# Optimization experiments

Hardware: AMD Instinct MI355X
Metric: run time of the kernel (lower is better)

The kernel has to match this reference:

```python
import jax, jax.numpy as jnp
import numpy as np

E, D, H, K = 8, 768, 3072, 2   # num_experts, embed_size, expert_size, top-k
TAU = 1.0
BN, PN = 32, 196

def l2norm(v):
    # F.normalize(p=2, dim=-1), eps=1e-12
    return v / jnp.maximum(jnp.linalg.norm(v, axis=-1, keepdims=True), 1e-12)

def setup_inputs() -> dict:
    key = jax.random.key(0)
    ks = jax.random.split(key, 8)
    s = 0.02  # weight init scale for stability
    return {
        "x": jax.random.normal(ks[0], (BN, PN, D), dtype=jnp.float32),
        "Wlinear": jax.random.normal(ks[1], (D, D), dtype=jnp.float32) * s,
        "learnedE": jax.random.normal(ks[2], (E, D), dtype=jnp.float32),
        "bias": jnp.zeros((BN * PN, E), dtype=jnp.float32),
        "W1": jax.random.normal(ks[3], (E, D, H), dtype=jnp.float32) * s,
        "b1": jnp.zeros((E, H), dtype=jnp.float32),
        "W2": jax.random.normal(ks[4], (E, H, D), dtype=jnp.float32) * s,
        "b2": jnp.zeros((E, D), dtype=jnp.float32),
        "sW1": jax.random.normal(ks[5], (D, H), dtype=jnp.float32) * s,
        "sb1": jnp.zeros((H,), dtype=jnp.float32),
        "sW2": jax.random.normal(ks[6], (H, D), dtype=jnp.float32) * s,
        "sb2": jnp.zeros((D,), dtype=jnp.float32),
    }

def reference(x, Wlinear, learnedE, bias, W1, b1, W2, b2, sW1, sb1, sW2, sb2):
    bn, pn, d = x.shape
    patches = x.reshape(bn * pn, d)                      # [T, D]
    proj = l2norm(patches @ Wlinear.T)                   # router projection
    routed = proj @ l2norm(learnedE).T                   # [T, E] cosine scores
    probs = jax.nn.softmax((routed + bias) / TAU, axis=1)  # eval path (no noise)
    k_probs, k_idx = jax.lax.top_k(probs, K)             # [T, K]
    # combine weights: scatter top-k probs into dense [T, E] gate matrix
    T = probs.shape[0]
    gates = jnp.zeros_like(probs).at[jnp.arange(T)[:, None], k_idx].add(k_probs)
    # expert MLPs computed densely for all experts, masked by gates
    h = jax.nn.gelu(jnp.einsum('td,edh->teh', patches, W1) + b1[None], approximate=False)
    eo = jnp.einsum('teh,ehd->ted', h, W2) + b2[None]    # [T, E, D]
    moe = jnp.einsum('ted,te->td', eo, gates)            # weighted combine
    # shared expert (expert_list[-1]) applied to every token; dropout is identity in eval
    shared = jax.nn.gelu(patches @ sW1 + sb1, approximate=False) @ sW2 + sb2
    return (moe + shared).reshape(bn, pn, d)
```

## Files before the change

kernel.cpp:

```cpp
#include <hip/hip_runtime.h>
#include <hip/hip_bf16.h>

typedef __hip_bfloat16 bf16;
typedef __attribute__((ext_vector_type(8))) short short8;
typedef __attribute__((ext_vector_type(4))) float f32x4;

#define T_TOK 6272
#define D_DIM 768
#define H_DIM 3072
#define NEXP 8
#define MAXTILES 160

__device__ __forceinline__ void async16(void* lds, const void* g) {
  __builtin_amdgcn_global_load_lds(
      (const __attribute__((address_space(1))) void*)g,
      (__attribute__((address_space(3))) void*)lds, 16, 0, 0);
}

__device__ __forceinline__ float gelu_f(float x) {
  float z = x * 0.70710678118654752f;
  float az = fabsf(z);
  float t = 1.f / (1.f + 0.3275911f * az);
  float poly = ((((1.061405429f * t - 1.453152027f) * t + 1.421413741f) * t -
                 0.284496736f) * t + 0.254829592f) * t;
  float e = __expf(-az * az);
  float er = 1.f - poly * e;
  er = copysignf(er, z);
  return 0.5f * x * (1.f + er);
}


__global__ void cast_hilo(const float* __restrict__ in, bf16* __restrict__ hi,
                          bf16* __restrict__ lo, int n) {
  int i = blockIdx.x * blockDim.x + threadIdx.x;
  int stride = gridDim.x * blockDim.x;
  for (; i < n; i += stride) {
    float x = in[i];
    bf16 h = __float2bfloat16(x);
    hi[i] = h;
    lo[i] = __float2bfloat16(x - __bfloat162float(h));
  }
}

__global__ void transpose_cast(const float* __restrict__ in, bf16* __restrict__ out,
                               int R, int C) {
  __shared__ float tile[32][33];
  int b = blockIdx.z;
  const float* ib = in + (size_t)b * R * C;
  bf16* ob = out + (size_t)b * R * C;
  int r0 = blockIdx.x * 32, c0 = blockIdx.y * 32;
  int tx = threadIdx.x & 31, ty = threadIdx.x >> 5;
  for (int i = 0; i < 32; i += 8)
    tile[ty + i][tx] = ib[(size_t)(r0 + ty + i) * C + c0 + tx];
  __syncthreads();
  for (int i = 0; i < 32; i += 8)
    ob[(size_t)(c0 + ty + i) * R + r0 + tx] = __float2bfloat16(tile[tx][ty + i]);
}

__global__ void norm_learnedE(const float* __restrict__ lE, float* __restrict__ eHat) {
  int wave = threadIdx.x >> 6, lane = threadIdx.x & 63;
  for (int e = wave; e < NEXP; e += 4) {
    float v[12];
    float ss = 0.f;
    for (int j = 0; j < 12; j++) {
      v[j] = lE[e * D_DIM + lane + 64 * j];
      ss += v[j] * v[j];
    }
    for (int o = 32; o; o >>= 1) ss += __shfl_xor(ss, o);
    float rn = 1.f / fmaxf(sqrtf(ss), 1e-12f);
    for (int j = 0; j < 12; j++) eHat[e * D_DIM + lane + 64 * j] = v[j] * rn;
  }
}


__global__ __launch_bounds__(256) void gemm_router(
    const bf16* __restrict__ pHi, const bf16* __restrict__ pLo,
    const bf16* __restrict__ wHi, const bf16* __restrict__ wLo,
    float* __restrict__ y) {
  __shared__ __align__(16) bf16 As[2][128 * 32];
  __shared__ __align__(16) bf16 Bs[2][128 * 32];
  int tid = threadIdx.x, wave = tid >> 6, lane = tid & 63;
  int wr = wave >> 1, wc = wave & 1;
  int rowbase = blockIdx.x * 128, colbase = blockIdx.y * 128;
  int sc8 = (lane & 3) * 8;

  size_t aoff[2], boff[2];
  for (int p = 0; p < 2; p++) {
    int r = wave * 32 + p * 16 + (lane >> 2);
    aoff[p] = (size_t)(rowbase + r) * D_DIM + sc8;
    boff[p] = (size_t)(colbase + r) * D_DIM + sc8;
  }

  auto stage = [&](int buf, int ks) {
    int term = ks / 24;
    const bf16* A = (term == 1) ? pLo : pHi;
    const bf16* B = (term == 2) ? wLo : wHi;
    int kk = (ks - term * 24) * 32;
#pragma unroll
    for (int p = 0; p < 2; p++) {
      async16(&As[buf][(wave * 32 + p * 16) * 32], A + aoff[p] + kk);
      async16(&Bs[buf][(wave * 32 + p * 16) * 32], B + boff[p] + kk);
    }
  };

  f32x4 acc[4][4];
#pragma unroll
  for (int m = 0; m < 4; m++)
#pragma unroll
    for (int n = 0; n < 4; n++) acc[m][n] = 0.f;

  stage(0, 0);
  __syncthreads();
  int cur = 0;
  for (int ks = 0; ks < 72; ks++) {
    if (ks < 71) stage(cur ^ 1, ks + 1);
    int koff = (lane >> 4) * 8;
    const bf16* Ac = As[cur];
    const bf16* Bc = Bs[cur];
    short8 af[4], bfr[4];
#pragma unroll
    for (int m = 0; m < 4; m++)
      af[m] = *(const short8*)&Ac[(wr * 64 + m * 16 + (lane & 15)) * 32 + koff];
#pragma unroll
    for (int n = 0; n < 4; n++)
      bfr[n] = *(const short8*)&Bc[(wc * 64 + n * 16 + (lane & 15)) * 32 + koff];
#pragma unroll
    for (int m = 0; m < 4; m++)
#pragma unroll
      for (int n = 0; n < 4; n++)
        acc[m][n] = __builtin_amdgcn_mfma_f32_16x16x32_bf16(af[m], bfr[n], acc[m][n], 0, 0, 0);
    __syncthreads();
    cur ^= 1;
  }
  for (int m = 0; m < 4; m++)
    for (int n = 0; n < 4; n++)
      for (int j = 0; j < 4; j++) {
        int r = rowbase + wr * 64 + m * 16 + (lane >> 4) * 4 + j;
        int c = colbase + wc * 64 + n * 16 + (lane & 15);
        y[(size_t)r * D_DIM + c] = acc[m][n][j];
      }
}


__global__ void router_epi(const float* __restrict__ y, const float* __restrict__ eHat,
                           const float* __restrict__ bias, int* __restrict__ gidx,
                           float* __restrict__ gval, int* __restrict__ counts) {
  int wave = threadIdx.x >> 6, lane = threadIdx.x & 63;
  int t = blockIdx.x * 4 + wave;
  float v[12];
  float ss = 0.f;
  for (int j = 0; j < 12; j++) {
    v[j] = y[(size_t)t * D_DIM + lane + 64 * j];
    ss += v[j] * v[j];
  }
  for (int o = 32; o; o >>= 1) ss += __shfl_xor(ss, o);
  float d[NEXP];
  for (int e = 0; e < NEXP; e++) {
    float s = 0.f;
    for (int j = 0; j < 12; j++) s += v[j] * eHat[e * D_DIM + lane + 64 * j];
    for (int o = 32; o; o >>= 1) s += __shfl_xor(s, o);
    d[e] = s;
  }
  if (lane == 0) {
    float rn = 1.f / fmaxf(sqrtf(ss), 1e-12f);
    float sc[NEXP], mx = -1e30f;
    for (int e = 0; e < NEXP; e++) {
      sc[e] = d[e] * rn + bias[t * NEXP + e];
      mx = fmaxf(mx, sc[e]);
    }
    float p[NEXP], sum = 0.f;
    for (int e = 0; e < NEXP; e++) {
      p[e] = expf(sc[e] - mx);
      sum += p[e];
    }
    float inv = 1.f / sum;
    int i1 = 0;
    for (int e = 1; e < NEXP; e++)
      if (sc[e] > sc[i1]) i1 = e;
    int i2 = -1;
    for (int e = 0; e < NEXP; e++) {
      if (e == i1) continue;
      if (i2 < 0 || sc[e] > sc[i2]) i2 = e;
    }
    gidx[t * 2] = i1;
    gidx[t * 2 + 1] = i2;
    gval[t * 2] = p[i1] * inv;
    gval[t * 2 + 1] = p[i2] * inv;
    atomicAdd(&counts[i1], 1);
    atomicAdd(&counts[i2], 1);
  }
}


__global__ void scan_build(const int* __restrict__ counts, int* __restrict__ segstart,
                           int* __restrict__ cursors, int* __restrict__ tiles,
                           int* __restrict__ numtiles) {
  if (threadIdx.x == 0) {
    int off = 0;
    for (int e = 0; e < NEXP; e++) {
      segstart[e] = off;
      cursors[e] = off;
      off += counts[e];
    }
    segstart[NEXP] = off;
    segstart[NEXP + 1] = off + T_TOK;
    int nt = 0;
    for (int e = 0; e < NEXP + 1; e++) {
      int cnt = (e < NEXP) ? counts[e] : T_TOK;
      int ntl = (cnt + 127) >> 7;
      for (int l = 0; l < ntl; l++) {
        tiles[nt * 2] = e;
        tiles[nt * 2 + 1] = l;
        nt++;
      }
    }
    *numtiles = nt;
  }
}

__global__ void fill_assign(const int* __restrict__ gidx, int* __restrict__ cursors,
                            int* __restrict__ rowtok, int* __restrict__ slot_of) {
  int t = blockIdx.x * 256 + threadIdx.x;
  if (t >= T_TOK) return;
  for (int k = 0; k < 2; k++) {
    int e = gidx[t * 2 + k];
    int pos = atomicAdd(&cursors[e], 1);
    rowtok[pos] = t;
    slot_of[t * 2 + k] = pos;
  }
  rowtok[2 * T_TOK + t] = t;
}


__global__ __launch_bounds__(256) void gemm_ffn1(
    const bf16* __restrict__ pHi, const bf16* __restrict__ W1T,
    const bf16* __restrict__ sW1T, const float* __restrict__ b1,
    const float* __restrict__ sb1, const int* __restrict__ segstart,
    const int* __restrict__ tiles, const int* __restrict__ numtiles,
    const int* __restrict__ rowtok, bf16* __restrict__ hbuf) {
  int gx = blockIdx.x;
  if (gx >= *numtiles) return;
  int seg = tiles[gx * 2], lt = tiles[gx * 2 + 1];
  int s0 = segstart[seg] + lt * 128;
  int send = segstart[seg + 1];
  const bf16* Bw = (seg < NEXP) ? W1T + (size_t)seg * H_DIM * D_DIM : sW1T;
  const float* bb = (seg < NEXP) ? b1 + seg * H_DIM : sb1;

  __shared__ __align__(16) bf16 As[2][128 * 32];
  __shared__ __align__(16) bf16 Bs[2][128 * 32];
  int tid = threadIdx.x, wave = tid >> 6, lane = tid & 63;
  int wr = wave >> 1, wc = wave & 1;
  int colbase = blockIdx.y * 128;
  int sc8 = (lane & 3) * 8;

  const bf16* arow[2];
  const bf16* brow[2];
  for (int p = 0; p < 2; p++) {
    int r = wave * 32 + p * 16 + (lane >> 2);
    int s = s0 + r;
    if (s > send - 1) s = send - 1;
    arow[p] = pHi + (size_t)rowtok[s] * D_DIM + sc8;
    brow[p] = Bw + (size_t)(colbase + r) * D_DIM + sc8;
  }

  auto stage = [&](int buf, int ks) {
    int kk = ks * 32;
#pragma unroll
    for (int p = 0; p < 2; p++) {
      async16(&As[buf][(wave * 32 + p * 16) * 32], arow[p] + kk);
      async16(&Bs[buf][(wave * 32 + p * 16) * 32], brow[p] + kk);
    }
  };

  f32x4 acc[4][4];
#pragma unroll
  for (int m = 0; m < 4; m++)
#pragma unroll
    for (int n = 0; n < 4; n++) acc[m][n] = 0.f;

  stage(0, 0);
  __syncthreads();
  int cur = 0;
  for (int ks = 0; ks < 24; ks++) {
    if (ks < 23) stage(cur ^ 1, ks + 1);
    int koff = (lane >> 4) * 8;
    const bf16* Ac = As[cur];
    const bf16* Bc = Bs[cur];
    short8 af[4], bfr[4];
#pragma unroll
    for (int m = 0; m < 4; m++)
      af[m] = *(const short8*)&Ac[(wr * 64 + m * 16 + (lane & 15)) * 32 + koff];
#pragma unroll
    for (int n = 0; n < 4; n++)
      bfr[n] = *(const short8*)&Bc[(wc * 64 + n * 16 + (lane & 15)) * 32 + koff];
#pragma unroll
    for (int m = 0; m < 4; m++)
#pragma unroll
      for (int n = 0; n < 4; n++)
        acc[m][n] = __builtin_amdgcn_mfma_f32_16x16x32_bf16(af[m], bfr[n], acc[m][n], 0, 0, 0);
    __syncthreads();
    cur ^= 1;
  }
#pragma unroll
  for (int n = 0; n < 4; n++) {
    int c = colbase + wc * 64 + n * 16 + (lane & 15);
    float bv = bb[c];
#pragma unroll
    for (int m = 0; m < 4; m++)
#pragma unroll
      for (int j = 0; j < 4; j++) {
        int s = s0 + wr * 64 + m * 16 + (lane >> 4) * 4 + j;
        if (s < send) {
          float xv = acc[m][n][j] + bv;
          hbuf[(size_t)s * H_DIM + c] = __float2bfloat16(gelu_f(xv));
        }
      }
  }
}


__global__ __launch_bounds__(256) void gemm_ffn2(
    const bf16* __restrict__ hbuf, const bf16* __restrict__ W2T,
    const bf16* __restrict__ sW2T, const float* __restrict__ b2,
    const float* __restrict__ sb2, const int* __restrict__ segstart,
    const int* __restrict__ tiles, const int* __restrict__ numtiles,
    float* __restrict__ moebuf) {
  int gx = blockIdx.x;
  if (gx >= *numtiles) return;
  int seg = tiles[gx * 2], lt = tiles[gx * 2 + 1];
  int s0 = segstart[seg] + lt * 128;
  int send = segstart[seg + 1];
  const bf16* Bw = (seg < NEXP) ? W2T + (size_t)seg * H_DIM * D_DIM : sW2T;
  const float* bb = (seg < NEXP) ? b2 + seg * D_DIM : sb2;

  __shared__ __align__(16) bf16 As[2][128 * 32];
  __shared__ __align__(16) bf16 Bs[2][128 * 32];
  int tid = threadIdx.x, wave = tid >> 6, lane = tid & 63;
  int wr = wave >> 1, wc = wave & 1;
  int colbase = blockIdx.y * 128;
  int sc8 = (lane & 3) * 8;

  const bf16* arow[2];
  const bf16* brow[2];
  for (int p = 0; p < 2; p++) {
    int r = wave * 32 + p * 16 + (lane >> 2);
    int s = s0 + r;
    if (s > send - 1) s = send - 1;
    arow[p] = hbuf + (size_t)s * H_DIM + sc8;
    brow[p] = Bw + (size_t)(colbase + r) * H_DIM + sc8;
  }

  auto stage = [&](int buf, int ks) {
    int kk = ks * 32;
#pragma unroll
    for (int p = 0; p < 2; p++) {
      async16(&As[buf][(wave * 32 + p * 16) * 32], arow[p] + kk);
      async16(&Bs[buf][(wave * 32 + p * 16) * 32], brow[p] + kk);
    }
  };

  f32x4 acc[4][4];
#pragma unroll
  for (int m = 0; m < 4; m++)
#pragma unroll
    for (int n = 0; n < 4; n++) acc[m][n] = 0.f;

  stage(0, 0);
  __syncthreads();
  int cur = 0;
  for (int ks = 0; ks < 96; ks++) {
    if (ks < 95) stage(cur ^ 1, ks + 1);
    int koff = (lane >> 4) * 8;
    const bf16* Ac = As[cur];
    const bf16* Bc = Bs[cur];
    short8 af[4], bfr[4];
#pragma unroll
    for (int m = 0; m < 4; m++)
      af[m] = *(const short8*)&Ac[(wr * 64 + m * 16 + (lane & 15)) * 32 + koff];
#pragma unroll
    for (int n = 0; n < 4; n++)
      bfr[n] = *(const short8*)&Bc[(wc * 64 + n * 16 + (lane & 15)) * 32 + koff];
#pragma unroll
    for (int m = 0; m < 4; m++)
#pragma unroll
      for (int n = 0; n < 4; n++)
        acc[m][n] = __builtin_amdgcn_mfma_f32_16x16x32_bf16(af[m], bfr[n], acc[m][n], 0, 0, 0);
    __syncthreads();
    cur ^= 1;
  }
#pragma unroll
  for (int n = 0; n < 4; n++) {
    int c = colbase + wc * 64 + n * 16 + (lane & 15);
    float bv = bb[c];
#pragma unroll
    for (int m = 0; m < 4; m++)
#pragma unroll
      for (int j = 0; j < 4; j++) {
        int s = s0 + wr * 64 + m * 16 + (lane >> 4) * 4 + j;
        if (s < send) moebuf[(size_t)s * D_DIM + c] = acc[m][n][j] + bv;
      }
  }
}


__global__ void combine_out(const float* __restrict__ moebuf, const float* __restrict__ gval,
                            const int* __restrict__ slot_of, float* __restrict__ out) {
  int i = blockIdx.x * 256 + threadIdx.x;
  const int total = T_TOK * (D_DIM / 4);
  if (i >= total) return;
  int t = i / (D_DIM / 4), c = i % (D_DIM / 4);
  float g0 = gval[2 * t], g1 = gval[2 * t + 1];
  int sA = slot_of[2 * t], sB = slot_of[2 * t + 1];
  const f32x4* pa = (const f32x4*)(moebuf + (size_t)sA * D_DIM) + c;
  const f32x4* pb = (const f32x4*)(moebuf + (size_t)sB * D_DIM) + c;
  const f32x4* ps = (const f32x4*)(moebuf + (size_t)(2 * T_TOK + t) * D_DIM) + c;
  f32x4 r = g0 * (*pa) + g1 * (*pb) + *ps;
  ((f32x4*)out)[i] = r;
}


extern "C" void kernel_launch(void* const* d_in, const int* in_sizes, int n_in,
                              void* d_out, int out_size, void* d_ws, size_t ws_size,
                              hipStream_t stream) {
  const float* x = (const float*)d_in[0];
  const float* Wlinear = (const float*)d_in[1];
  const float* learnedE = (const float*)d_in[2];
  const float* bias = (const float*)d_in[3];
  const float* W1 = (const float*)d_in[4];
  const float* b1 = (const float*)d_in[5];
  const float* W2 = (const float*)d_in[6];
  const float* b2 = (const float*)d_in[7];
  const float* sW1 = (const float*)d_in[8];
  const float* sb1 = (const float*)d_in[9];
  const float* sW2 = (const float*)d_in[10];
  const float* sb2 = (const float*)d_in[11];
  float* out = (float*)d_out;

  char* ws = (char*)d_ws;
  size_t off = 0;
  auto alloc = [&](size_t bytes) {
    char* p = ws + off;
    off += (bytes + 255) & ~(size_t)255;
    return p;
  };
  float* eHat = (float*)alloc(8 * 768 * 4);
  bf16* pHi = (bf16*)alloc((size_t)T_TOK * D_DIM * 2);
  bf16* pLo = (bf16*)alloc((size_t)T_TOK * D_DIM * 2);
  bf16* wHi = (bf16*)alloc((size_t)D_DIM * D_DIM * 2);
  bf16* wLo = (bf16*)alloc((size_t)D_DIM * D_DIM * 2);
  bf16* W1T = (bf16*)alloc((size_t)NEXP * D_DIM * H_DIM * 2);
  bf16* W2T = (bf16*)alloc((size_t)NEXP * D_DIM * H_DIM * 2);
  bf16* sW1T = (bf16*)alloc((size_t)D_DIM * H_DIM * 2);
  bf16* sW2T = (bf16*)alloc((size_t)D_DIM * H_DIM * 2);
  float* y = (float*)alloc((size_t)T_TOK * D_DIM * 4);
  bf16* hbuf = (bf16*)alloc((size_t)3 * T_TOK * H_DIM * 2);
  float* moebuf = (float*)alloc((size_t)3 * T_TOK * D_DIM * 4);
  int* gidx = (int*)alloc(T_TOK * 2 * 4);
  float* gval = (float*)alloc(T_TOK * 2 * 4);
  int* rowtok = (int*)alloc(3 * T_TOK * 4);
  int* slot_of = (int*)alloc(T_TOK * 2 * 4);
  int* counts = (int*)alloc(8 * 4);
  int* segstart = (int*)alloc(10 * 4);
  int* cursors = (int*)alloc(8 * 4);
  int* numtiles = (int*)alloc(4);
  int* tiles = (int*)alloc(MAXTILES * 2 * 4);
  (void)ws_size; (void)in_sizes; (void)n_in; (void)out_size;

  hipMemsetAsync(counts, 0, 8 * 4, stream);
  norm_learnedE<<<1, 256, 0, stream>>>(learnedE, eHat);
  cast_hilo<<<2048, 256, 0, stream>>>(x, pHi, pLo, T_TOK * D_DIM);
  cast_hilo<<<1024, 256, 0, stream>>>(Wlinear, wHi, wLo, D_DIM * D_DIM);
  transpose_cast<<<dim3(D_DIM / 32, H_DIM / 32, NEXP), 256, 0, stream>>>(W1, W1T, D_DIM, H_DIM);
  transpose_cast<<<dim3(H_DIM / 32, D_DIM / 32, NEXP), 256, 0, stream>>>(W2, W2T, H_DIM, D_DIM);
  transpose_cast<<<dim3(D_DIM / 32, H_DIM / 32, 1), 256, 0, stream>>>(sW1, sW1T, D_DIM, H_DIM);
  transpose_cast<<<dim3(H_DIM / 32, D_DIM / 32, 1), 256, 0, stream>>>(sW2, sW2T, H_DIM, D_DIM);

  gemm_router<<<dim3(T_TOK / 128, D_DIM / 128), 256, 0, stream>>>(pHi, pLo, wHi, wLo, y);
  router_epi<<<T_TOK / 4, 256, 0, stream>>>(y, eHat, bias, gidx, gval, counts);
  scan_build<<<1, 64, 0, stream>>>(counts, segstart, cursors, tiles, numtiles);
  fill_assign<<<(T_TOK + 255) / 256, 256, 0, stream>>>(gidx, cursors, rowtok, slot_of);

  gemm_ffn1<<<dim3(MAXTILES, H_DIM / 128), 256, 0, stream>>>(
      pHi, W1T, sW1T, b1, sb1, segstart, tiles, numtiles, rowtok, hbuf);
  gemm_ffn2<<<dim3(MAXTILES, D_DIM / 128), 256, 0, stream>>>(
      hbuf, W2T, sW2T, b2, sb2, segstart, tiles, numtiles, moebuf);

  combine_out<<<(T_TOK * (D_DIM / 4) + 255) / 256, 256, 0, stream>>>(moebuf, gval, slot_of, out);
}
```

Measured before the change: 797.0 us.

## Double K-tile to 64 with XOR-swizzled LDS layout in all GEMMs

Raises the K depth per pipeline stage from 32 to 64 in the router, FFN1 and FFN2 GEMMs, which halves the number of barriers and stage iterations. Global-to-LDS loads now write rows of 64 elements with an XOR swizzle on the 16-byte slot index, and fragment reads apply the same swizzle to avoid LDS bank conflicts. Launch bounds request 2 blocks per CU. LDS use per block doubles to 64KB, which may limit occupancy.

```diff
diff --git a/kernel.cpp b/kernel.cpp
--- a/kernel.cpp
+++ b/kernel.cpp
@@ -10,6 +10,7 @@
 #define H_DIM 3072
 #define NEXP 8
 #define MAXTILES 160
+#define BK 64
 
 __device__ __forceinline__ void async16(void* lds, const void* g) {
   __builtin_amdgcn_global_load_lds(
@@ -73,33 +74,34 @@
 }
 
 
-__global__ __launch_bounds__(256) void gemm_router(
+__global__ __launch_bounds__(256, 2) void gemm_router(
     const bf16* __restrict__ pHi, const bf16* __restrict__ pLo,
     const bf16* __restrict__ wHi, const bf16* __restrict__ wLo,
     float* __restrict__ y) {
-  __shared__ __align__(16) bf16 As[2][128 * 32];
-  __shared__ __align__(16) bf16 Bs[2][128 * 32];
+  __shared__ __align__(16) bf16 As[2][128 * BK];
+  __shared__ __align__(16) bf16 Bs[2][128 * BK];
   int tid = threadIdx.x, wave = tid >> 6, lane = tid & 63;
   int wr = wave >> 1, wc = wave & 1;
   int rowbase = blockIdx.x * 128, colbase = blockIdx.y * 128;
-  int sc8 = (lane & 3) * 8;
-
-  size_t aoff[2], boff[2];
-  for (int p = 0; p < 2; p++) {
-    int r = wave * 32 + p * 16 + (lane >> 2);
-    aoff[p] = (size_t)(rowbase + r) * D_DIM + sc8;
-    boff[p] = (size_t)(colbase + r) * D_DIM + sc8;
+  int rslot = (lane & 7) ^ (lane >> 3);
+
+  size_t aoff[4], boff[4];
+#pragma unroll
+  for (int c = 0; c < 4; c++) {
+    int row = 32 * wave + 8 * c + (lane >> 3);
+    aoff[c] = (size_t)(rowbase + row) * D_DIM + rslot * 8;
+    boff[c] = (size_t)(colbase + row) * D_DIM + rslot * 8;
   }
 
   auto stage = [&](int buf, int ks) {
-    int term = ks / 24;
+    int term = ks / 12;
     const bf16* A = (term == 1) ? pLo : pHi;
     const bf16* B = (term == 2) ? wLo : wHi;
-    int kk = (ks - term * 24) * 32;
-#pragma unroll
-    for (int p = 0; p < 2; p++) {
-      async16(&As[buf][(wave * 32 + p * 16) * 32], A + aoff[p] + kk);
-      async16(&Bs[buf][(wave * 32 + p * 16) * 32], B + boff[p] + kk);
+    int kk = (ks - term * 12) * BK;
+#pragma unroll
+    for (int c = 0; c < 4; c++) {
+      async16(&As[buf][(32 * wave + 8 * c) * BK], A + aoff[c] + kk);
+      async16(&Bs[buf][(32 * wave + 8 * c) * BK], B + boff[c] + kk);
     }
   };
 
@@ -112,23 +114,32 @@
   stage(0, 0);
   __syncthreads();
   int cur = 0;
-  for (int ks = 0; ks < 72; ks++) {
-    if (ks < 71) stage(cur ^ 1, ks + 1);
-    int koff = (lane >> 4) * 8;
+  int q = lane >> 4, fr = lane & 15;
+  for (int ks = 0; ks < 36; ks++) {
+    if (ks < 35) stage(cur ^ 1, ks + 1);
     const bf16* Ac = As[cur];
     const bf16* Bc = Bs[cur];
-    short8 af[4], bfr[4];
-#pragma unroll
-    for (int m = 0; m < 4; m++)
-      af[m] = *(const short8*)&Ac[(wr * 64 + m * 16 + (lane & 15)) * 32 + koff];
-#pragma unroll
-    for (int n = 0; n < 4; n++)
-      bfr[n] = *(const short8*)&Bc[(wc * 64 + n * 16 + (lane & 15)) * 32 + koff];
-#pragma unroll
-    for (int m = 0; m < 4; m++)
-#pragma unroll
-      for (int n = 0; n < 4; n++)
-        acc[m][n] = __builtin_amdgcn_mfma_f32_16x16x32_bf16(af[m], bfr[n], acc[m][n], 0, 0, 0);
+#pragma unroll
+    for (int kh = 0; kh < 2; kh++) {
+      short8 af[4], bfr[4];
+#pragma unroll
+      for (int m = 0; m < 4; m++) {
+        int row = wr * 64 + m * 16 + fr;
+        int ls = ((kh << 2) + q) ^ (row & 7);
+        af[m] = *(const short8*)&Ac[row * BK + ls * 8];
+      }
+#pragma unroll
+      for (int n = 0; n < 4; n++) {
+        int row = wc * 64 + n * 16 + fr;
+        int ls = ((kh << 2) + q) ^ (row & 7);
+        bfr[n] = *(const short8*)&Bc[row * BK + ls * 8];
+      }
+#pragma unroll
+      for (int m = 0; m < 4; m++)
+#pragma unroll
+        for (int n = 0; n < 4; n++)
+          acc[m][n] = __builtin_amdgcn_mfma_f32_16x16x32_bf16(af[m], bfr[n], acc[m][n], 0, 0, 0);
+    }
     __syncthreads();
     cur ^= 1;
   }
@@ -232,7 +243,7 @@
 }
 
 
-__global__ __launch_bounds__(256) void gemm_ffn1(
+__global__ __launch_bounds__(256, 2) void gemm_ffn1(
     const bf16* __restrict__ pHi, const bf16* __restrict__ W1T,
     const bf16* __restrict__ sW1T, const float* __restrict__ b1,
     const float* __restrict__ sb1, const int* __restrict__ segstart,
@@ -246,29 +257,30 @@
   const bf16* Bw = (seg < NEXP) ? W1T + (size_t)seg * H_DIM * D_DIM : sW1T;
   const float* bb = (seg < NEXP) ? b1 + seg * H_DIM : sb1;
 
-  __shared__ __align__(16) bf16 As[2][128 * 32];
-  __shared__ __align__(16) bf16 Bs[2][128 * 32];
+  __shared__ __align__(16) bf16 As[2][128 * BK];
+  __shared__ __align__(16) bf16 Bs[2][128 * BK];
   int tid = threadIdx.x, wave = tid >> 6, lane = tid & 63;
   int wr = wave >> 1, wc = wave & 1;
   int colbase = blockIdx.y * 128;
-  int sc8 = (lane & 3) * 8;
-
-  const bf16* arow[2];
-  const bf16* brow[2];
-  for (int p = 0; p < 2; p++) {
-    int r = wave * 32 + p * 16 + (lane >> 2);
-    int s = s0 + r;
+  int rslot = (lane & 7) ^ (lane >> 3);
+
+  const bf16* aptr[4];
+  const bf16* bptr[4];
+#pragma unroll
+  for (int c = 0; c < 4; c++) {
+    int row = 32 * wave + 8 * c + (lane >> 3);
+    int s = s0 + row;
     if (s > send - 1) s = send - 1;
-    arow[p] = pHi + (size_t)rowtok[s] * D_DIM + sc8;
-    brow[p] = Bw + (size_t)(colbase + r) * D_DIM + sc8;
+    aptr[c] = pHi + (size_t)rowtok[s] * D_DIM + rslot * 8;
+    bptr[c] = Bw + (size_t)(colbase + row) * D_DIM + rslot * 8;
   }
 
   auto stage = [&](int buf, int ks) {
-    int kk = ks * 32;
-#pragma unroll
-    for (int p = 0; p < 2; p++) {
-      async16(&As[buf][(wave * 32 + p * 16) * 32], arow[p] + kk);
-      async16(&Bs[buf][(wave * 32 + p * 16) * 32], brow[p] + kk);
+    int kk = ks * BK;
+#pragma unroll
+    for (int c = 0; c < 4; c++) {
+      async16(&As[buf][(32 * wave + 8 * c) * BK], aptr[c] + kk);
+      async16(&Bs[buf][(32 * wave + 8 * c) * BK], bptr[c] + kk);
     }
   };
 
@@ -281,23 +293,32 @@
   stage(0, 0);
   __syncthreads();
   int cur = 0;
-  for (int ks = 0; ks < 24; ks++) {
-    if (ks < 23) stage(cur ^ 1, ks + 1);
-    int koff = (lane >> 4) * 8;
+  int q = lane >> 4, fr = lane & 15;
+  for (int ks = 0; ks < 12; ks++) {
+    if (ks < 11) stage(cur ^ 1, ks + 1);
     const bf16* Ac = As[cur];
     const bf16* Bc = Bs[cur];
-    short8 af[4], bfr[4];
-#pragma unroll
-    for (int m = 0; m < 4; m++)
-      af[m] = *(const short8*)&Ac[(wr * 64 + m * 16 + (lane & 15)) * 32 + koff];
-#pragma unroll
-    for (int n = 0; n < 4; n++)
-      bfr[n] = *(const short8*)&Bc[(wc * 64 + n * 16 + (lane & 15)) * 32 + koff];
-#pragma unroll
-    for (int m = 0; m < 4; m++)
-#pragma unroll
-      for (int n = 0; n < 4; n++)
-        acc[m][n] = __builtin_amdgcn_mfma_f32_16x16x32_bf16(af[m], bfr[n], acc[m][n], 0, 0, 0);
+#pragma unroll
+    for (int kh = 0; kh < 2; kh++) {
+      short8 af[4], bfr[4];
+#pragma unroll
+      for (int m = 0; m < 4; m++) {
+        int row = wr * 64 + m * 16 + fr;
+        int ls = ((kh << 2) + q) ^ (row & 7);
+        af[m] = *(const short8*)&Ac[row * BK + ls * 8];
+      }
+#pragma unroll
+      for (int n = 0; n < 4; n++) {
+        int row = wc * 64 + n * 16 + fr;
+        int ls = ((kh << 2) + q) ^ (row & 7);
+        bfr[n] = *(const short8*)&Bc[row * BK + ls * 8];
+      }
+#pragma unroll
+      for (int m = 0; m < 4; m++)
+#pragma unroll
+        for (int n = 0; n < 4; n++)
+          acc[m][n] = __builtin_amdgcn_mfma_f32_16x16x32_bf16(af[m], bfr[n], acc[m][n], 0, 0, 0);
+    }
     __syncthreads();
     cur ^= 1;
   }
@@ -319,7 +340,7 @@
 }
 
 
-__global__ __launch_bounds__(256) void gemm_ffn2(
+__global__ __launch_bounds__(256, 2) void gemm_ffn2(
     const bf16* __restrict__ hbuf, const bf16* __restrict__ W2T,
     const bf16* __restrict__ sW2T, const float* __restrict__ b2,
     const float* __restrict__ sb2, const int* __restrict__ segstart,
@@ -333,29 +354,30 @@
   const bf16* Bw = (seg < NEXP) ? W2T + (size_t)seg * H_DIM * D_DIM : sW2T;
   const float* bb = (seg < NEXP) ? b2 + seg * D_DIM : sb2;
 
-  __shared__ __align__(16) bf16 As[2][128 * 32];
-  __shared__ __align__(16) bf16 Bs[2][128 * 32];
+  __shared__ __align__(16) bf16 As[2][128 * BK];
+  __shared__ __align__(16) bf16 Bs[2][128 * BK];
   int tid = threadIdx.x, wave = tid >> 6, lane = tid & 63;
   int wr = wave >> 1, wc = wave & 1;
   int colbase = blockIdx.y * 128;
-  int sc8 = (lane & 3) * 8;
-
-  const bf16* arow[2];
-  const bf16* brow[2];
-  for (int p = 0; p < 2; p++) {
-    int r = wave * 32 + p * 16 + (lane >> 2);
-    int s = s0 + r;
+  int rslot = (lane & 7) ^ (lane >> 3);
+
+  const bf16* aptr[4];
+  const bf16* bptr[4];
+#pragma unroll
+  for (int c = 0; c < 4; c++) {
+    int row = 32 * wave + 8 * c + (lane >> 3);
+    int s = s0 + row;
     if (s > send - 1) s = send - 1;
-    arow[p] = hbuf + (size_t)s * H_DIM + sc8;
-    brow[p] = Bw + (size_t)(colbase + r) * H_DIM + sc8;
+    aptr[c] = hbuf + (size_t)s * H_DIM + rslot * 8;
+    bptr[c] = Bw + (size_t)(colbase + row) * H_DIM + rslot * 8;
   }
 
   auto stage = [&](int buf, int ks) {
-    int kk = ks * 32;
-#pragma unroll
-    for (int p = 0; p < 2; p++) {
-      async16(&As[buf][(wave * 32 + p * 16) * 32], arow[p] + kk);
-      async16(&Bs[buf][(wave * 32 + p * 16) * 32], brow[p] + kk);
+    int kk = ks * BK;
+#pragma unroll
+    for (int c = 0; c < 4; c++) {
+      async16(&As[buf][(32 * wave + 8 * c) * BK], aptr[c] + kk);
+      async16(&Bs[buf][(32 * wave + 8 * c) * BK], bptr[c] + kk);
     }
   };
 
@@ -368,23 +390,32 @@
   stage(0, 0);
   __syncthreads();
   int cur = 0;
-  for (int ks = 0; ks < 96; ks++) {
-    if (ks < 95) stage(cur ^ 1, ks + 1);
-    int koff = (lane >> 4) * 8;
+  int q = lane >> 4, fr = lane & 15;
+  for (int ks = 0; ks < 48; ks++) {
+    if (ks < 47) stage(cur ^ 1, ks + 1);
     const bf16* Ac = As[cur];
     const bf16* Bc = Bs[cur];
-    short8 af[4], bfr[4];
-#pragma unroll
-    for (int m = 0; m < 4; m++)
-      af[m] = *(const short8*)&Ac[(wr * 64 + m * 16 + (lane & 15)) * 32 + koff];
-#pragma unroll
-    for (int n = 0; n < 4; n++)
-      bfr[n] = *(const short8*)&Bc[(wc * 64 + n * 16 + (lane & 15)) * 32 + koff];
-#pragma unroll
-    for (int m = 0; m < 4; m++)
-#pragma unroll
-      for (int n = 0; n < 4; n++)
-        acc[m][n] = __builtin_amdgcn_mfma_f32_16x16x32_bf16(af[m], bfr[n], acc[m][n], 0, 0, 0);
+#pragma unroll
+    for (int kh = 0; kh < 2; kh++) {
+      short8 af[4], bfr[4];
+#pragma unroll
+      for (int m = 0; m < 4; m++) {
+        int row = wr * 64 + m * 16 + fr;
+        int ls = ((kh << 2) + q) ^ (row & 7);
+        af[m] = *(const short8*)&Ac[row * BK + ls * 8];
+      }
+#pragma unroll
+      for (int n = 0; n < 4; n++) {
+        int row = wc * 64 + n * 16 + fr;
+        int ls = ((kh << 2) + q) ^ (row & 7);
+        bfr[n] = *(const short8*)&Bc[row * BK + ls * 8];
+      }
+#pragma unroll
+      for (int m = 0; m < 4; m++)
+#pragma unroll
+        for (int n = 0; n < 4; n++)
+          acc[m][n] = __builtin_amdgcn_mfma_f32_16x16x32_bf16(af[m], bfr[n], acc[m][n], 0, 0, 0);
+    }
     __syncthreads();
     cur ^= 1;
   }
```

Measured after the change: 780.6 us. 1.02x faster.

## Swizzle LDS layouts and deepen GEMM pipelines with explicit waitcnt barriers

Applied to the files above, without the earlier changes.

Applies XOR swizzles to the LDS tile layouts in the router and FFN GEMMs to cut bank conflicts. The router GEMM moves to a K-tile of 64 with a swizzled 8-slot layout. The FFN GEMMs replace __syncthreads with explicit vmcnt/lgkmcnt waits and raw barriers, so two stages stay in flight, and they raise MFMA priority with setprio. Launch bounds are tightened to allow more occupancy, which may increase register pressure, and the hand-written waitcnt counts must match the number of outstanding async loads.

```diff
diff --git a/kernel.cpp b/kernel.cpp
--- a/kernel.cpp
+++ b/kernel.cpp
@@ -10,6 +10,12 @@
 #define H_DIM 3072
 #define NEXP 8
 #define MAXTILES 160
+#define BKR 64
+
+#define S_BARRIER() __builtin_amdgcn_s_barrier()
+#define WAIT_VM4() asm volatile("s_waitcnt vmcnt(4)" ::: "memory")
+#define WAIT_VM0() asm volatile("s_waitcnt vmcnt(0)" ::: "memory")
+#define WAIT_LGKM0() asm volatile("s_waitcnt lgkmcnt(0)" ::: "memory")
 
 __device__ __forceinline__ void async16(void* lds, const void* g) {
   __builtin_amdgcn_global_load_lds(
@@ -73,33 +79,34 @@
 }
 
 
-__global__ __launch_bounds__(256) void gemm_router(
+__global__ __launch_bounds__(256, 2) void gemm_router(
     const bf16* __restrict__ pHi, const bf16* __restrict__ pLo,
     const bf16* __restrict__ wHi, const bf16* __restrict__ wLo,
     float* __restrict__ y) {
-  __shared__ __align__(16) bf16 As[2][128 * 32];
-  __shared__ __align__(16) bf16 Bs[2][128 * 32];
+  __shared__ __align__(16) bf16 As[2][128 * BKR];
+  __shared__ __align__(16) bf16 Bs[2][128 * BKR];
   int tid = threadIdx.x, wave = tid >> 6, lane = tid & 63;
   int wr = wave >> 1, wc = wave & 1;
   int rowbase = blockIdx.x * 128, colbase = blockIdx.y * 128;
-  int sc8 = (lane & 3) * 8;
-
-  size_t aoff[2], boff[2];
-  for (int p = 0; p < 2; p++) {
-    int r = wave * 32 + p * 16 + (lane >> 2);
-    aoff[p] = (size_t)(rowbase + r) * D_DIM + sc8;
-    boff[p] = (size_t)(colbase + r) * D_DIM + sc8;
+  int rslot = (lane & 7) ^ (lane >> 3);
+
+  size_t aoff[4], boff[4];
+#pragma unroll
+  for (int c = 0; c < 4; c++) {
+    int row = 32 * wave + 8 * c + (lane >> 3);
+    aoff[c] = (size_t)(rowbase + row) * D_DIM + rslot * 8;
+    boff[c] = (size_t)(colbase + row) * D_DIM + rslot * 8;
   }
 
   auto stage = [&](int buf, int ks) {
-    int term = ks / 24;
+    int term = ks / 12;
     const bf16* A = (term == 1) ? pLo : pHi;
     const bf16* B = (term == 2) ? wLo : wHi;
-    int kk = (ks - term * 24) * 32;
-#pragma unroll
-    for (int p = 0; p < 2; p++) {
-      async16(&As[buf][(wave * 32 + p * 16) * 32], A + aoff[p] + kk);
-      async16(&Bs[buf][(wave * 32 + p * 16) * 32], B + boff[p] + kk);
+    int kk = (ks - term * 12) * BKR;
+#pragma unroll
+    for (int c = 0; c < 4; c++) {
+      async16(&As[buf][(32 * wave + 8 * c) * BKR], A + aoff[c] + kk);
+      async16(&Bs[buf][(32 * wave + 8 * c) * BKR], B + boff[c] + kk);
     }
   };
 
@@ -112,23 +119,32 @@
   stage(0, 0);
   __syncthreads();
   int cur = 0;
-  for (int ks = 0; ks < 72; ks++) {
-    if (ks < 71) stage(cur ^ 1, ks + 1);
-    int koff = (lane >> 4) * 8;
+  int q = lane >> 4, fr = lane & 15;
+  for (int ks = 0; ks < 36; ks++) {
+    if (ks < 35) stage(cur ^ 1, ks + 1);
     const bf16* Ac = As[cur];
     const bf16* Bc = Bs[cur];
-    short8 af[4], bfr[4];
-#pragma unroll
-    for (int m = 0; m < 4; m++)
-      af[m] = *(const short8*)&Ac[(wr * 64 + m * 16 + (lane & 15)) * 32 + koff];
-#pragma unroll
-    for (int n = 0; n < 4; n++)
-      bfr[n] = *(const short8*)&Bc[(wc * 64 + n * 16 + (lane & 15)) * 32 + koff];
-#pragma unroll
-    for (int m = 0; m < 4; m++)
-#pragma unroll
-      for (int n = 0; n < 4; n++)
-        acc[m][n] = __builtin_amdgcn_mfma_f32_16x16x32_bf16(af[m], bfr[n], acc[m][n], 0, 0, 0);
+#pragma unroll
+    for (int kh = 0; kh < 2; kh++) {
+      short8 af[4], bfr[4];
+#pragma unroll
+      for (int m = 0; m < 4; m++) {
+        int row = wr * 64 + m * 16 + fr;
+        int ls = ((kh << 2) + q) ^ (row & 7);
+        af[m] = *(const short8*)&Ac[row * BKR + ls * 8];
+      }
+#pragma unroll
+      for (int n = 0; n < 4; n++) {
+        int row = wc * 64 + n * 16 + fr;
+        int ls = ((kh << 2) + q) ^ (row & 7);
+        bfr[n] = *(const short8*)&Bc[row * BKR + ls * 8];
+      }
+#pragma unroll
+      for (int m = 0; m < 4; m++)
+#pragma unroll
+        for (int n = 0; n < 4; n++)
+          acc[m][n] = __builtin_amdgcn_mfma_f32_16x16x32_bf16(af[m], bfr[n], acc[m][n], 0, 0, 0);
+    }
     __syncthreads();
     cur ^= 1;
   }
@@ -232,7 +248,8 @@
 }
 
 
-__global__ __launch_bounds__(256) void gemm_ffn1(
+
+__global__ __launch_bounds__(256, 4) void gemm_ffn1(
     const bf16* __restrict__ pHi, const bf16* __restrict__ W1T,
     const bf16* __restrict__ sW1T, const float* __restrict__ b1,
     const float* __restrict__ sb1, const int* __restrict__ segstart,
@@ -251,24 +268,25 @@
   int tid = threadIdx.x, wave = tid >> 6, lane = tid & 63;
   int wr = wave >> 1, wc = wave & 1;
   int colbase = blockIdx.y * 128;
-  int sc8 = (lane & 3) * 8;
-
-  const bf16* arow[2];
-  const bf16* brow[2];
+  int g8 = (((lane & 3) ^ ((lane >> 3) & 3))) * 8;
+
+  const bf16* aptr[2];
+  const bf16* bptr[2];
+#pragma unroll
   for (int p = 0; p < 2; p++) {
     int r = wave * 32 + p * 16 + (lane >> 2);
     int s = s0 + r;
     if (s > send - 1) s = send - 1;
-    arow[p] = pHi + (size_t)rowtok[s] * D_DIM + sc8;
-    brow[p] = Bw + (size_t)(colbase + r) * D_DIM + sc8;
+    aptr[p] = pHi + (size_t)rowtok[s] * D_DIM + g8;
+    bptr[p] = Bw + (size_t)(colbase + r) * D_DIM + g8;
   }
 
   auto stage = [&](int buf, int ks) {
     int kk = ks * 32;
 #pragma unroll
     for (int p = 0; p < 2; p++) {
-      async16(&As[buf][(wave * 32 + p * 16) * 32], arow[p] + kk);
-      async16(&Bs[buf][(wave * 32 + p * 16) * 32], brow[p] + kk);
+      async16(&As[buf][(wave * 32 + p * 16) * 32], aptr[p] + kk);
+      async16(&Bs[buf][(wave * 32 + p * 16) * 32], bptr[p] + kk);
     }
   };
 
@@ -278,28 +296,36 @@
 #pragma unroll
     for (int n = 0; n < 4; n++) acc[m][n] = 0.f;
 
+  WAIT_VM0();
   stage(0, 0);
-  __syncthreads();
-  int cur = 0;
-  for (int ks = 0; ks < 24; ks++) {
-    if (ks < 23) stage(cur ^ 1, ks + 1);
-    int koff = (lane >> 4) * 8;
-    const bf16* Ac = As[cur];
-    const bf16* Bc = Bs[cur];
+  stage(1, 1);
+
+  int q = lane >> 4, fr = lane & 15;
+  int ls8 = (q ^ ((fr >> 1) & 3)) * 8;
+
+#define NT1 24
+  for (int ks = 0; ks < NT1; ks++) {
+    if (ks + 1 < NT1) { WAIT_VM4(); } else { WAIT_VM0(); }
+    S_BARRIER();
+    const bf16* Ac = As[ks & 1];
+    const bf16* Bc = Bs[ks & 1];
     short8 af[4], bfr[4];
 #pragma unroll
     for (int m = 0; m < 4; m++)
-      af[m] = *(const short8*)&Ac[(wr * 64 + m * 16 + (lane & 15)) * 32 + koff];
+      af[m] = *(const short8*)&Ac[(wr * 64 + m * 16 + fr) * 32 + ls8];
 #pragma unroll
     for (int n = 0; n < 4; n++)
-      bfr[n] = *(const short8*)&Bc[(wc * 64 + n * 16 + (lane & 15)) * 32 + koff];
+      bfr[n] = *(const short8*)&Bc[(wc * 64 + n * 16 + fr) * 32 + ls8];
+    __builtin_amdgcn_s_setprio(1);
 #pragma unroll
     for (int m = 0; m < 4; m++)
 #pragma unroll
       for (int n = 0; n < 4; n++)
         acc[m][n] = __builtin_amdgcn_mfma_f32_16x16x32_bf16(af[m], bfr[n], acc[m][n], 0, 0, 0);
-    __syncthreads();
-    cur ^= 1;
+    __builtin_amdgcn_s_setprio(0);
+    WAIT_LGKM0();
+    S_BARRIER();
+    if (ks + 2 < NT1) stage(ks & 1, ks + 2);
   }
 #pragma unroll
   for (int n = 0; n < 4; n++) {
@@ -319,7 +345,7 @@
 }
 
 
-__global__ __launch_bounds__(256) void gemm_ffn2(
+__global__ __launch_bounds__(256, 4) void gemm_ffn2(
     const bf16* __restrict__ hbuf, const bf16* __restrict__ W2T,
     const bf16* __restrict__ sW2T, const float* __restrict__ b2,
     const float* __restrict__ sb2, const int* __restrict__ segstart,
@@ -338,24 +364,25 @@
   int tid = threadIdx.x, wave = tid >> 6, lane = tid & 63;
   int wr = wave >> 1, wc = wave & 1;
   int colbase = blockIdx.y * 128;
-  int sc8 = (lane & 3) * 8;
-
-  const bf16* arow[2];
-  const bf16* brow[2];
+  int g8 = (((lane & 3) ^ ((lane >> 3) & 3))) * 8;
+
+  const bf16* aptr[2];
+  const bf16* bptr[2];
+#pragma unroll
   for (int p = 0; p < 2; p++) {
     int r = wave * 32 + p * 16 + (lane >> 2);
     int s = s0 + r;
     if (s > send - 1) s = send - 1;
-    arow[p] = hbuf + (size_t)s * H_DIM + sc8;
-    brow[p] = Bw + (size_t)(colbase + r) * H_DIM + sc8;
+    aptr[p] = hbuf + (size_t)s * H_DIM + g8;
+    bptr[p] = Bw + (size_t)(colbase + r) * H_DIM + g8;
   }
 
   auto stage = [&](int buf, int ks) {
     int kk = ks * 32;
 #pragma unroll
     for (int p = 0; p < 2; p++) {
-      async16(&As[buf][(wave * 32 + p * 16) * 32], arow[p] + kk);
-      async16(&Bs[buf][(wave * 32 + p * 16) * 32], brow[p] + kk);
+      async16(&As[buf][(wave * 32 + p * 16) * 32], aptr[p] + kk);
+      async16(&Bs[buf][(wave * 32 + p * 16) * 32], bptr[p] + kk);
     }
   };
 
@@ -365,28 +392,36 @@
 #pragma unroll
     for (int n = 0; n < 4; n++) acc[m][n] = 0.f;
 
+  WAIT_VM0();
   stage(0, 0);
-  __syncthreads();
-  int cur = 0;
-  for (int ks = 0; ks < 96; ks++) {
-    if (ks < 95) stage(cur ^ 1, ks + 1);
-    int koff = (lane >> 4) * 8;
-    const bf16* Ac = As[cur];
-    const bf16* Bc = Bs[cur];
+  stage(1, 1);
+
+  int q = lane >> 4, fr = lane & 15;
+  int ls8 = (q ^ ((fr >> 1) & 3)) * 8;
+
+#define NT2 96
+  for (int ks = 0; ks < NT2; ks++) {
+    if (ks + 1 < NT2) { WAIT_VM4(); } else { WAIT_VM0(); }
+    S_BARRIER();
+    const bf16* Ac = As[ks & 1];
+    const bf16* Bc = Bs[ks & 1];
     short8 af[4], bfr[4];
 #pragma unroll
     for (int m = 0; m < 4; m++)
-      af[m] = *(const short8*)&Ac[(wr * 64 + m * 16 + (lane & 15)) * 32 + koff];
+      af[m] = *(const short8*)&Ac[(wr * 64 + m * 16 + fr) * 32 + ls8];
 #pragma unroll
     for (int n = 0; n < 4; n++)
-      bfr[n] = *(const short8*)&Bc[(wc * 64 + n * 16 + (lane & 15)) * 32 + koff];
+      bfr[n] = *(const short8*)&Bc[(wc * 64 + n * 16 + fr) * 32 + ls8];
+    __builtin_amdgcn_s_setprio(1);
 #pragma unroll
     for (int m = 0; m < 4; m++)
 #pragma unroll
       for (int n = 0; n < 4; n++)
         acc[m][n] = __builtin_amdgcn_mfma_f32_16x16x32_bf16(af[m], bfr[n], acc[m][n], 0, 0, 0);
-    __syncthreads();
-    cur ^= 1;
+    __builtin_amdgcn_s_setprio(0);
+    WAIT_LGKM0();
+    S_BARRIER();
+    if (ks + 2 < NT2) stage(ks & 1, ks + 2);
   }
 #pragma unroll
   for (int n = 0; n < 4; n++) {
```

Measured after the change: 723.1 us. -9.3%, faster.
